# Kernel tuning notes

Hardware: AMD Instinct MI355X
Metric: run time of the kernel (lower is better)

## Reference

```python
import jax, jax.numpy as jnp
import numpy as np

TEMP = 1.0


def _layernorm(x):
    # mean/std over last dim; torch.std is unbiased (ddof=1); no eps in original
    x = x - jnp.mean(x, axis=-1, keepdims=True)
    return x / jnp.std(x, axis=-1, keepdims=True, ddof=1)


def setup_inputs() -> dict:
    key = jax.random.key(0)
    ks = jax.random.split(key, 5)
    B, S, d_in, d = 8, 2048, 768, 1024
    return {
        "seq": jax.random.normal(ks[0], (B, S, d_in), dtype=jnp.float32),
        "embedding": jax.random.normal(ks[1], (d_in, d), dtype=jnp.float32),
        "W1": jax.random.normal(ks[2], (d, d), dtype=jnp.float32),
        "W2": jax.random.normal(ks[3], (d, d), dtype=jnp.float32),
        "readout": jax.random.normal(ks[4], (d,), dtype=jnp.float32),
    }


def reference(seq, embedding, W1, W2, readout):
    d_in = seq.shape[-1]
    d = embedding.shape[-1]
    x = jnp.matmul(seq, embedding) / jnp.sqrt(jnp.float32(d_in))  # [B,S,d]
    # depth == 1: single block
    gram = jnp.einsum("bsd,btd->bst", x, x) / x.shape[-1]  # [B,S,S]
    weights = jax.nn.softmax(gram / TEMP, axis=-1)
    post_attn = _layernorm(x + jnp.matmul(weights, x))  # [B,S,d]
    h = jnp.matmul(post_attn, W1) / jnp.sqrt(jnp.float32(d))
    h = jnp.matmul(jax.nn.relu(h), W2) / jnp.sqrt(jnp.float32(d))
    x = _layernorm(h + post_attn)
    pooled = jnp.mean(x, axis=1)  # [B,d]
    out = jnp.matmul(pooled, readout) / jnp.sqrt(jnp.float32(d))  # [B]
    return out
```

## Files before the change

kernel.cpp:

```cpp
#include <hip/hip_runtime.h>
#include <hip/hip_bf16.h>

typedef __bf16 bf16x8 __attribute__((ext_vector_type(8)));
typedef float f32x4 __attribute__((ext_vector_type(4)));

__device__ __forceinline__ unsigned short f2bf(float f) {
  union { float f; unsigned u; } x; x.f = f;
  unsigned r = x.u + 0x7fffu + ((x.u >> 16) & 1u);
  return (unsigned short)(r >> 16);
}
__device__ __forceinline__ float bf2f(unsigned short u) {
  union { unsigned u; float f; } x; x.u = (unsigned)u << 16;
  return x.f;
}
__device__ __forceinline__ unsigned short f2h(float f) {
  union { _Float16 h; unsigned short u; } x; x.h = (_Float16)f;
  return x.u;
}
__device__ __forceinline__ float h2f(unsigned short u) {
  union { _Float16 h; unsigned short u; } x; x.u = u;
  return (float)x.h;
}

__device__ __forceinline__ void async_ld16(const void* g, void* l) {
  __builtin_amdgcn_global_load_lds(
      (__attribute__((address_space(1))) void*)const_cast<void*>(g),
      (__attribute__((address_space(3))) void*)l, 16, 0, 0);
}


#define EPI_F32    0
#define EPI_BF     1
#define EPI_RELUBF 2
#define EPI_F16    3

__global__ __launch_bounds__(512, 2) void gemm_bt(
    const unsigned short* __restrict__ A,
    const unsigned short* __restrict__ Bt,
    int M, int N, int K, int nbatch,
    long sA, long sB, long sC,
    float scale, int mode, void* __restrict__ outp)
{
  __shared__ unsigned short lds[65536];
  const int t = threadIdx.x;
  const int w = t >> 6, l = t & 63;
  const int lr = l & 15, lg = l >> 4;
  const int wr = w >> 2, wc = w & 3;
  const int ntn = N >> 8;
  const int tiles = (M >> 8) * ntn;
  const int chunk = (tiles * nbatch) >> 3;
  const int bid = blockIdx.x;
  const int wg = (bid & 7) * chunk + (bid >> 3);
  const int batch = wg / tiles;
  const int rem = wg - batch * tiles;
  const int row0 = (rem / ntn) << 8;
  const int col0 = (rem % ntn) << 8;

  const unsigned short* Ab  = A  + (long)batch * sA;
  const unsigned short* Btb = Bt + (long)batch * sB;

  const int ks = ((lg ^ ((lr >> 1) & 3)) << 3);

  const int srow = w * 16 + (l >> 2);
  const int kgo  = (((l & 3) ^ ((l >> 3) & 3)) << 3);
  const long aoff0 = (long)(row0 + srow) * K + kgo;
  const long boff0 = (long)(col0 + srow) * K + kgo;
  const long off128 = (long)K << 7;

  const int NT = K >> 6;

#define STAGEP(partE, base, kcol)                                      \
  { async_ld16((base) + (kcol),          &lds[(partE) + t * 8]);       \
    async_ld16((base) + off128 + (kcol), &lds[(partE) + 4096 + t * 8]); }

  f32x4 acc[8][4];
#pragma unroll
  for (int m = 0; m < 8; ++m)
#pragma unroll
    for (int n = 0; n < 4; ++n) acc[m][n] = (f32x4){0.f, 0.f, 0.f, 0.f};

  STAGEP(0,     Btb + boff0, 0);
  STAGEP(8192,  Ab + aoff0,  0);
  STAGEP(16384, Btb + boff0, 32);
  STAGEP(24576, Ab + aoff0,  32);
  __builtin_amdgcn_sched_barrier(0);

  for (int tt = 0; tt < NT; ++tt) {
    const int bufe  = (tt & 1) << 15;
    const int nbufe = ((tt + 1) & 1) << 15;
    const bool st = (tt + 1) < NT;
    const int kn = (tt + 1) << 6;

#pragma unroll
    for (int kh = 0; kh < 2; ++kh) {
      if (kh == 0 || st) { asm volatile("s_waitcnt vmcnt(4)" ::: "memory"); }
      else               { asm volatile("s_waitcnt vmcnt(0)" ::: "memory"); }
      __builtin_amdgcn_sched_barrier(0);
      __builtin_amdgcn_s_barrier();
      __builtin_amdgcn_sched_barrier(0);

      const int pB = bufe + kh * 16384;
      const int pA = pB + 8192;

      bf16x8 bfr[4];
#pragma unroll
      for (int nf = 0; nf < 4; ++nf) {
        int rb = wc * 64 + nf * 16 + lr;
        bfr[nf] = *(const bf16x8*)&lds[pB + rb * 32 + ks];
      }
      {
        bf16x8 af[4];
#pragma unroll
        for (int i = 0; i < 4; ++i) {
          int ra = wr * 128 + i * 16 + lr;
          af[i] = *(const bf16x8*)&lds[pA + ra * 32 + ks];
        }
        if (st) STAGEP(nbufe + kh * 16384, Btb + boff0, kn + kh * 32);
        __builtin_amdgcn_s_setprio(1);
#pragma unroll
        for (int i = 0; i < 4; ++i)
#pragma unroll
          for (int nf = 0; nf < 4; ++nf)
            acc[i][nf] = __builtin_amdgcn_mfma_f32_16x16x32_bf16(af[i], bfr[nf], acc[i][nf], 0, 0, 0);
        __builtin_amdgcn_s_setprio(0);
      }
      {
        bf16x8 af[4];
#pragma unroll
        for (int i = 0; i < 4; ++i) {
          int ra = wr * 128 + 64 + i * 16 + lr;
          af[i] = *(const bf16x8*)&lds[pA + ra * 32 + ks];
        }
        if (st) STAGEP(nbufe + kh * 16384 + 8192, Ab + aoff0, kn + kh * 32);
        __builtin_amdgcn_s_setprio(1);
#pragma unroll
        for (int i = 0; i < 4; ++i)
#pragma unroll
          for (int nf = 0; nf < 4; ++nf)
            acc[4 + i][nf] = __builtin_amdgcn_mfma_f32_16x16x32_bf16(af[i], bfr[nf], acc[4 + i][nf], 0, 0, 0);
        __builtin_amdgcn_s_setprio(0);
      }
      __builtin_amdgcn_sched_barrier(0);
    }
  }

  float* outF = (float*)outp;
  unsigned short* outH = (unsigned short*)outp;
  const size_t cb = (size_t)batch * (size_t)sC;
#pragma unroll
  for (int mf = 0; mf < 8; ++mf) {
    int rbase = row0 + wr * 128 + mf * 16 + lg * 4;
#pragma unroll
    for (int nf = 0; nf < 4; ++nf) {
      int c = col0 + wc * 64 + nf * 16 + lr;
      f32x4 v = acc[mf][nf];
#pragma unroll
      for (int q = 0; q < 4; ++q) {
        size_t idx = cb + (size_t)(rbase + q) * N + c;
        float val = v[q] * scale;
        if (mode == EPI_F32)         outF[idx] = val;
        else if (mode == EPI_BF)     outH[idx] = f2bf(val);
        else if (mode == EPI_RELUBF) outH[idx] = f2bf(fmaxf(val, 0.f));
        else                         outH[idx] = f2h(val);
      }
    }
  }
#undef STAGEP
}

__global__ __launch_bounds__(512, 2) void gram_sym(
    const unsigned short* __restrict__ X,
    unsigned short* __restrict__ outH)
{
  __shared__ unsigned short lds[65536];
  const int t = threadIdx.x;
  const int w = t >> 6, l = t & 63;
  const int lr = l & 15, lg = l >> 4;
  const int wr = w >> 2, wc = w & 3;
  const int bid = blockIdx.x;
  const int wg = (bid & 7) * 36 + (bid >> 3);
  const int batch = wg / 36;
  int r8 = wg - batch * 36;
  int bi = 0;
  while (r8 >= 8 - bi) { r8 -= 8 - bi; ++bi; }
  const int bj = bi + r8;
  const int row0 = bi << 8;
  const int col0 = bj << 8;

  const unsigned short* Xb = X + (long)batch * 2048 * 1024;

  const int ks = ((lg ^ ((lr >> 1) & 3)) << 3);
  const int srow = w * 16 + (l >> 2);
  const int kgo  = (((l & 3) ^ ((l >> 3) & 3)) << 3);
  const long aoff0 = (long)(row0 + srow) * 1024 + kgo;
  const long boff0 = (long)(col0 + srow) * 1024 + kgo;
  const long off128 = 1024L << 7;

#define STAGEP(partE, base, kcol)                                      \
  { async_ld16((base) + (kcol),          &lds[(partE) + t * 8]);       \
    async_ld16((base) + off128 + (kcol), &lds[(partE) + 4096 + t * 8]); }

  f32x4 acc[8][4];
#pragma unroll
  for (int m = 0; m < 8; ++m)
#pragma unroll
    for (int n = 0; n < 4; ++n) acc[m][n] = (f32x4){0.f, 0.f, 0.f, 0.f};

  STAGEP(0,     Xb + boff0, 0);
  STAGEP(8192,  Xb + aoff0,  0);
  STAGEP(16384, Xb + boff0, 32);
  STAGEP(24576, Xb + aoff0,  32);
  __builtin_amdgcn_sched_barrier(0);

  for (int tt = 0; tt < 16; ++tt) {
    const int bufe  = (tt & 1) << 15;
    const int nbufe = ((tt + 1) & 1) << 15;
    const bool st = (tt + 1) < 16;
    const int kn = (tt + 1) << 6;

#pragma unroll
    for (int kh = 0; kh < 2; ++kh) {
      if (kh == 0 || st) { asm volatile("s_waitcnt vmcnt(4)" ::: "memory"); }
      else               { asm volatile("s_waitcnt vmcnt(0)" ::: "memory"); }
      __builtin_amdgcn_sched_barrier(0);
      __builtin_amdgcn_s_barrier();
      __builtin_amdgcn_sched_barrier(0);

      const int pB = bufe + kh * 16384;
      const int pA = pB + 8192;

      bf16x8 bfr[4];
#pragma unroll
      for (int nf = 0; nf < 4; ++nf) {
        int rb = wc * 64 + nf * 16 + lr;
        bfr[nf] = *(const bf16x8*)&lds[pB + rb * 32 + ks];
      }
      {
        bf16x8 af[4];
#pragma unroll
        for (int i = 0; i < 4; ++i) {
          int ra = wr * 128 + i * 16 + lr;
          af[i] = *(const bf16x8*)&lds[pA + ra * 32 + ks];
        }
        if (st) STAGEP(nbufe + kh * 16384, Xb + boff0, kn + kh * 32);
        __builtin_amdgcn_s_setprio(1);
#pragma unroll
        for (int i = 0; i < 4; ++i)
#pragma unroll
          for (int nf = 0; nf < 4; ++nf)
            acc[i][nf] = __builtin_amdgcn_mfma_f32_16x16x32_bf16(af[i], bfr[nf], acc[i][nf], 0, 0, 0);
        __builtin_amdgcn_s_setprio(0);
      }
      {
        bf16x8 af[4];
#pragma unroll
        for (int i = 0; i < 4; ++i) {
          int ra = wr * 128 + 64 + i * 16 + lr;
          af[i] = *(const bf16x8*)&lds[pA + ra * 32 + ks];
        }
        if (st) STAGEP(nbufe + kh * 16384 + 8192, Xb + aoff0, kn + kh * 32);
        __builtin_amdgcn_s_setprio(1);
#pragma unroll
        for (int i = 0; i < 4; ++i)
#pragma unroll
          for (int nf = 0; nf < 4; ++nf)
            acc[4 + i][nf] = __builtin_amdgcn_mfma_f32_16x16x32_bf16(af[i], bfr[nf], acc[4 + i][nf], 0, 0, 0);
        __builtin_amdgcn_s_setprio(0);
      }
      __builtin_amdgcn_sched_barrier(0);
    }
  }

  unsigned short* ob = outH + (size_t)batch * 2048 * 2048;
  const float scale = 1.0f / 1024.0f;
  const bool mirror = (bi != bj);
#pragma unroll
  for (int mf = 0; mf < 8; ++mf) {
    int rbase = row0 + wr * 128 + mf * 16 + lg * 4;
#pragma unroll
    for (int nf = 0; nf < 4; ++nf) {
      int c = col0 + wc * 64 + nf * 16 + lr;
      f32x4 v = acc[mf][nf];
      unsigned short h0 = f2h(v[0] * scale), h1 = f2h(v[1] * scale);
      unsigned short h2 = f2h(v[2] * scale), h3 = f2h(v[3] * scale);
      ob[(size_t)(rbase + 0) * 2048 + c] = h0;
      ob[(size_t)(rbase + 1) * 2048 + c] = h1;
      ob[(size_t)(rbase + 2) * 2048 + c] = h2;
      ob[(size_t)(rbase + 3) * 2048 + c] = h3;
      if (mirror) {
        ushort4 m4 = {h0, h1, h2, h3};
        *(ushort4*)&ob[(size_t)c * 2048 + rbase] = m4;
      }
    }
  }
#undef STAGEP
}


__device__ __forceinline__ float wave_sum(float v) {
#pragma unroll
  for (int o = 32; o; o >>= 1) v += __shfl_xor(v, o, 64);
  return v;
}
__device__ __forceinline__ float wave_max(float v) {
#pragma unroll
  for (int o = 32; o; o >>= 1) v = fmaxf(v, __shfl_xor(v, o, 64));
  return v;
}

__global__ __launch_bounds__(256) void cast_bf16(const float* __restrict__ in,
                                                 unsigned short* __restrict__ out, long n) {
  long i = ((long)blockIdx.x * 256 + threadIdx.x) * 4;
  if (i >= n) return;
  float4 v = *(const float4*)&in[i];
  ushort4 o;
  o.x = f2bf(v.x); o.y = f2bf(v.y); o.z = f2bf(v.z); o.w = f2bf(v.w);
  *(ushort4*)&out[i] = o;
}

__global__ __launch_bounds__(256) void transpose_cast(const float* __restrict__ in,
                                                      unsigned short* __restrict__ out,
                                                      int R, int C) {
  __shared__ float tile[32][33];
  int c0 = blockIdx.x * 32, r0 = blockIdx.y * 32;
  int tx = threadIdx.x, ty = threadIdx.y;
  for (int i = ty; i < 32; i += 8) tile[i][tx] = in[(size_t)(r0 + i) * C + c0 + tx];
  __syncthreads();
  for (int i = ty; i < 32; i += 8) out[(size_t)(c0 + i) * R + r0 + tx] = f2bf(tile[tx][i]);
}

__global__ __launch_bounds__(256) void transpose_b16(const unsigned short* __restrict__ in,
                                                     unsigned short* __restrict__ out,
                                                     int R, int C) {
  __shared__ unsigned short tile[32][33];
  int c0 = blockIdx.x * 32, r0 = blockIdx.y * 32;
  size_t zb = (size_t)blockIdx.z * R * C;
  int tx = threadIdx.x, ty = threadIdx.y;
  for (int i = ty; i < 32; i += 8) tile[i][tx] = in[zb + (size_t)(r0 + i) * C + c0 + tx];
  __syncthreads();
  for (int i = ty; i < 32; i += 8) out[zb + (size_t)(c0 + i) * R + r0 + tx] = tile[tx][i];
}

__global__ __launch_bounds__(256) void softmax_rows(const unsigned short* __restrict__ g,
                                                    unsigned short* __restrict__ wout) {
  __shared__ float red[4];
  int row = blockIdx.x, t = threadIdx.x;
  const unsigned short* gr = g + ((size_t)row << 11) + t * 8;
  ushort4 ua = *(const ushort4*)gr;
  ushort4 ub = *(const ushort4*)(gr + 4);
  float a0 = h2f(ua.x), a1 = h2f(ua.y), a2 = h2f(ua.z), a3 = h2f(ua.w);
  float b0 = h2f(ub.x), b1 = h2f(ub.y), b2 = h2f(ub.z), b3 = h2f(ub.w);
  float mx = fmaxf(fmaxf(fmaxf(a0, a1), fmaxf(a2, a3)),
                   fmaxf(fmaxf(b0, b1), fmaxf(b2, b3)));
  mx = wave_max(mx);
  if ((t & 63) == 0) red[t >> 6] = mx;
  __syncthreads();
  mx = fmaxf(fmaxf(red[0], red[1]), fmaxf(red[2], red[3]));
  float e0 = __expf(a0 - mx), e1 = __expf(a1 - mx), e2 = __expf(a2 - mx), e3 = __expf(a3 - mx);
  float e4 = __expf(b0 - mx), e5 = __expf(b1 - mx), e6 = __expf(b2 - mx), e7 = __expf(b3 - mx);
  float s = ((e0 + e1) + (e2 + e3)) + ((e4 + e5) + (e6 + e7));
  s = wave_sum(s);
  __syncthreads();
  if ((t & 63) == 0) red[t >> 6] = s;
  __syncthreads();
  s = (red[0] + red[1]) + (red[2] + red[3]);
  float inv = 1.0f / s;
  ushort4 o0, o1;
  o0.x = f2bf(e0 * inv); o0.y = f2bf(e1 * inv); o0.z = f2bf(e2 * inv); o0.w = f2bf(e3 * inv);
  o1.x = f2bf(e4 * inv); o1.y = f2bf(e5 * inv); o1.z = f2bf(e6 * inv); o1.w = f2bf(e7 * inv);
  size_t base = ((size_t)row << 11) + t * 8;
  *(ushort4*)&wout[base] = o0;
  *(ushort4*)&wout[base + 4] = o1;
}

__global__ __launch_bounds__(256) void ln_residual_bb(const unsigned short* __restrict__ xb,
                                                      const unsigned short* __restrict__ ab,
                                                      unsigned short* __restrict__ outB) {
  __shared__ float red[4];
  int row = blockIdx.x, t = threadIdx.x;
  size_t base = ((size_t)row << 10) + t * 4;
  ushort4 ua = *(const ushort4*)&xb[base];
  ushort4 ub = *(const ushort4*)&ab[base];
  float4 v = {bf2f(ua.x) + bf2f(ub.x), bf2f(ua.y) + bf2f(ub.y),
              bf2f(ua.z) + bf2f(ub.z), bf2f(ua.w) + bf2f(ub.w)};
  float s = (v.x + v.y) + (v.z + v.w);
  float ss = (v.x * v.x + v.y * v.y) + (v.z * v.z + v.w * v.w);
  s = wave_sum(s);
  if ((t & 63) == 0) red[t >> 6] = s;
  __syncthreads();
  s = (red[0] + red[1]) + (red[2] + red[3]);
  ss = wave_sum(ss);
  __syncthreads();
  if ((t & 63) == 0) red[t >> 6] = ss;
  __syncthreads();
  ss = (red[0] + red[1]) + (red[2] + red[3]);
  float mean = s * (1.0f / 1024.0f);
  float var = (ss - s * mean) * (1.0f / 1023.0f);
  float rstd = rsqrtf(var);
  ushort4 ob;
  ob.x = f2bf((v.x - mean) * rstd); ob.y = f2bf((v.y - mean) * rstd);
  ob.z = f2bf((v.z - mean) * rstd); ob.w = f2bf((v.w - mean) * rstd);
  *(ushort4*)&outB[base] = ob;
}

__global__ __launch_bounds__(256) void ln_residual_dot(const unsigned short* __restrict__ h2,
                                                       const unsigned short* __restrict__ post,
                                                       const float* __restrict__ readout,
                                                       float* __restrict__ rowdot) {
  __shared__ float red[4];
  int row = blockIdx.x, t = threadIdx.x;
  size_t base = ((size_t)row << 10) + t * 4;
  ushort4 ua = *(const ushort4*)&h2[base];
  ushort4 ub = *(const ushort4*)&post[base];
  float4 v = {bf2f(ua.x) + bf2f(ub.x), bf2f(ua.y) + bf2f(ub.y),
              bf2f(ua.z) + bf2f(ub.z), bf2f(ua.w) + bf2f(ub.w)};
  float s = (v.x + v.y) + (v.z + v.w);
  float ss = (v.x * v.x + v.y * v.y) + (v.z * v.z + v.w * v.w);
  s = wave_sum(s);
  if ((t & 63) == 0) red[t >> 6] = s;
  __syncthreads();
  s = (red[0] + red[1]) + (red[2] + red[3]);
  ss = wave_sum(ss);
  __syncthreads();
  if ((t & 63) == 0) red[t >> 6] = ss;
  __syncthreads();
  ss = (red[0] + red[1]) + (red[2] + red[3]);
  float mean = s * (1.0f / 1024.0f);
  float var = (ss - s * mean) * (1.0f / 1023.0f);
  float rstd = rsqrtf(var);
  float4 r = *(const float4*)&readout[t * 4];
  float dot = (v.x - mean) * rstd * r.x + (v.y - mean) * rstd * r.y +
              (v.z - mean) * rstd * r.z + (v.w - mean) * rstd * r.w;
  dot = wave_sum(dot);
  __syncthreads();
  if ((t & 63) == 0) red[t >> 6] = dot;
  __syncthreads();
  if (t == 0) rowdot[row] = (red[0] + red[1]) + (red[2] + red[3]);
}

__global__ __launch_bounds__(256) void reduce_out(const float* __restrict__ rowdot,
                                                  float* __restrict__ out) {
  __shared__ float red[4];
  int b = blockIdx.x, t = threadIdx.x;
  float s = 0.f;
  for (int i = t; i < 2048; i += 256) s += rowdot[(size_t)b * 2048 + i];
  s = wave_sum(s);
  if ((t & 63) == 0) red[t >> 6] = s;
  __syncthreads();
  if (t == 0) out[b] = ((red[0] + red[1]) + (red[2] + red[3])) * (1.0f / 65536.0f);
}

extern "C" void kernel_launch(void* const* d_in, const int* in_sizes, int n_in,
                              void* d_out, int out_size, void* d_ws, size_t ws_size,
                              hipStream_t stream) {
  const float* seq     = (const float*)d_in[0];
  const float* emb     = (const float*)d_in[1];
  const float* W1      = (const float*)d_in[2];
  const float* W2      = (const float*)d_in[3];
  const float* readout = (const float*)d_in[4];
  float* out = (float*)d_out;

  char* ws = (char*)d_ws;
  const size_t MB = 1024u * 1024u;
  unsigned short* x_b    = (unsigned short*)(ws + 0);
  unsigned short* h2b    = (unsigned short*)(ws + 0);
  unsigned short* xT     = (unsigned short*)(ws + 32 * MB);
  unsigned short* hrelu  = (unsigned short*)(ws + 32 * MB);
  unsigned short* gram   = (unsigned short*)(ws + 64 * MB);
  unsigned short* attn_b = (unsigned short*)(ws + 64 * MB);
  unsigned short* wts    = (unsigned short*)(ws + 128 * MB);
  unsigned short* post_b = (unsigned short*)(ws + 128 * MB);
  unsigned short* seq_b  = (unsigned short*)(ws + 192 * MB);
  unsigned short* embT   = (unsigned short*)(ws + 216 * MB);
  unsigned short* W1T    = (unsigned short*)(ws + 218 * MB);
  unsigned short* W2T    = (unsigned short*)(ws + 220 * MB);
  float*          rowdot = (float*)(ws + 222 * MB);

  cast_bf16<<<12288, 256, 0, stream>>>(seq, seq_b, 12582912L);
  transpose_cast<<<dim3(32, 24), dim3(32, 8), 0, stream>>>(emb, embT, 768, 1024);
  transpose_cast<<<dim3(32, 32), dim3(32, 8), 0, stream>>>(W1, W1T, 1024, 1024);
  transpose_cast<<<dim3(32, 32), dim3(32, 8), 0, stream>>>(W2, W2T, 1024, 1024);

  gemm_bt<<<256, 512, 0, stream>>>(seq_b, embT, 16384, 1024, 768, 1, 0, 0, 0,
                                   0.03608439182435161f, EPI_BF, x_b);

  transpose_b16<<<dim3(32, 64, 8), dim3(32, 8), 0, stream>>>(x_b, xT, 2048, 1024);

  gram_sym<<<288, 512, 0, stream>>>(x_b, gram);

  softmax_rows<<<16384, 256, 0, stream>>>(gram, wts);

  gemm_bt<<<256, 512, 0, stream>>>(wts, xT, 2048, 1024, 2048, 8,
                                   2048L * 2048, 1024L * 2048, 2048L * 1024,
                                   1.0f, EPI_BF, attn_b);

  ln_residual_bb<<<16384, 256, 0, stream>>>(x_b, attn_b, post_b);

  gemm_bt<<<256, 512, 0, stream>>>(post_b, W1T, 16384, 1024, 1024, 1, 0, 0, 0,
                                   0.03125f, EPI_RELUBF, hrelu);
  gemm_bt<<<256, 512, 0, stream>>>(hrelu, W2T, 16384, 1024, 1024, 1, 0, 0, 0,
                                   0.03125f, EPI_BF, h2b);

  ln_residual_dot<<<16384, 256, 0, stream>>>(h2b, post_b, readout, rowdot);
  reduce_out<<<8, 256, 0, stream>>>(rowdot, out);
}
```

Measured before the change: 368.5 us.

## Fuse fp32-to-bf16 cast into embedding GEMM and retile symmetric gram kernel

```diff
diff --git a/kernel.cpp b/kernel.cpp
--- a/kernel.cpp
+++ b/kernel.cpp
@@ -28,6 +28,7 @@
       (__attribute__((address_space(3))) void*)l, 16, 0, 0);
 }
 
+#define SB __builtin_amdgcn_sched_barrier(0)
 
 #define EPI_F32    0
 #define EPI_BF     1
@@ -60,7 +61,6 @@
   const unsigned short* Btb = Bt + (long)batch * sB;
 
   const int ks = ((lg ^ ((lr >> 1) & 3)) << 3);
-
   const int srow = w * 16 + (l >> 2);
   const int kgo  = (((l & 3) ^ ((l >> 3) & 3)) << 3);
   const long aoff0 = (long)(row0 + srow) * K + kgo;
@@ -83,7 +83,7 @@
   STAGEP(8192,  Ab + aoff0,  0);
   STAGEP(16384, Btb + boff0, 32);
   STAGEP(24576, Ab + aoff0,  32);
-  __builtin_amdgcn_sched_barrier(0);
+  SB;
 
   for (int tt = 0; tt < NT; ++tt) {
     const int bufe  = (tt & 1) << 15;
@@ -95,9 +95,9 @@
     for (int kh = 0; kh < 2; ++kh) {
       if (kh == 0 || st) { asm volatile("s_waitcnt vmcnt(4)" ::: "memory"); }
       else               { asm volatile("s_waitcnt vmcnt(0)" ::: "memory"); }
-      __builtin_amdgcn_sched_barrier(0);
+      SB;
       __builtin_amdgcn_s_barrier();
-      __builtin_amdgcn_sched_barrier(0);
+      SB;
 
       const int pB = bufe + kh * 16384;
       const int pA = pB + 8192;
@@ -140,7 +140,7 @@
             acc[4 + i][nf] = __builtin_amdgcn_mfma_f32_16x16x32_bf16(af[i], bfr[nf], acc[4 + i][nf], 0, 0, 0);
         __builtin_amdgcn_s_setprio(0);
       }
-      __builtin_amdgcn_sched_barrier(0);
+      SB;
     }
   }
 
@@ -168,37 +168,46 @@
 #undef STAGEP
 }
 
-__global__ __launch_bounds__(512, 2) void gram_sym(
-    const unsigned short* __restrict__ X,
-    unsigned short* __restrict__ outH)
+__global__ __launch_bounds__(512, 2) void g1_fused(
+    const float* __restrict__ A,
+    const unsigned short* __restrict__ Bt,
+    float scale, unsigned short* __restrict__ outB)
 {
   __shared__ unsigned short lds[65536];
   const int t = threadIdx.x;
   const int w = t >> 6, l = t & 63;
   const int lr = l & 15, lg = l >> 4;
   const int wr = w >> 2, wc = w & 3;
+  const int K = 768;
   const int bid = blockIdx.x;
-  const int wg = (bid & 7) * 36 + (bid >> 3);
-  const int batch = wg / 36;
-  int r8 = wg - batch * 36;
-  int bi = 0;
-  while (r8 >= 8 - bi) { r8 -= 8 - bi; ++bi; }
-  const int bj = bi + r8;
-  const int row0 = bi << 8;
-  const int col0 = bj << 8;
-
-  const unsigned short* Xb = X + (long)batch * 2048 * 1024;
+  const int wg = (bid & 7) * 32 + (bid >> 3);
+  const int row0 = (wg >> 2) << 8;
+  const int col0 = (wg & 3) << 8;
 
   const int ks = ((lg ^ ((lr >> 1) & 3)) << 3);
   const int srow = w * 16 + (l >> 2);
   const int kgo  = (((l & 3) ^ ((l >> 3) & 3)) << 3);
-  const long aoff0 = (long)(row0 + srow) * 1024 + kgo;
-  const long boff0 = (long)(col0 + srow) * 1024 + kgo;
-  const long off128 = 1024L << 7;
-
-#define STAGEP(partE, base, kcol)                                      \
-  { async_ld16((base) + (kcol),          &lds[(partE) + t * 8]);       \
-    async_ld16((base) + off128 + (kcol), &lds[(partE) + 4096 + t * 8]); }
+  const long ar0 = (long)(row0 + srow) * K + kgo;
+  const long ar1 = ar0 + (long)128 * K;
+  const long boff0 = (long)(col0 + srow) * K + kgo;
+  const long off128 = (long)K << 7;
+  const int NT = 12;
+
+#define STAGEB(partE, kcol)                                              \
+  { async_ld16(Bt + boff0 + (kcol),          &lds[(partE) + t * 8]);     \
+    async_ld16(Bt + boff0 + off128 + (kcol), &lds[(partE) + 4096 + t * 8]); }
+#define WRA(partE, q0, q1, q2, q3)                                       \
+  { uint4 pk;                                                            \
+    pk.x = (unsigned)f2bf(q0.x) | ((unsigned)f2bf(q0.y) << 16);          \
+    pk.y = (unsigned)f2bf(q0.z) | ((unsigned)f2bf(q0.w) << 16);          \
+    pk.z = (unsigned)f2bf(q1.x) | ((unsigned)f2bf(q1.y) << 16);          \
+    pk.w = (unsigned)f2bf(q1.z) | ((unsigned)f2bf(q1.w) << 16);          \
+    *(uint4*)&lds[(partE) + t * 8] = pk;                                 \
+    pk.x = (unsigned)f2bf(q2.x) | ((unsigned)f2bf(q2.y) << 16);          \
+    pk.y = (unsigned)f2bf(q2.z) | ((unsigned)f2bf(q2.w) << 16);          \
+    pk.z = (unsigned)f2bf(q3.x) | ((unsigned)f2bf(q3.y) << 16);          \
+    pk.w = (unsigned)f2bf(q3.z) | ((unsigned)f2bf(q3.w) << 16);          \
+    *(uint4*)&lds[(partE) + 4096 + t * 8] = pk; }
 
   f32x4 acc[8][4];
 #pragma unroll
@@ -206,25 +215,31 @@
 #pragma unroll
     for (int n = 0; n < 4; ++n) acc[m][n] = (f32x4){0.f, 0.f, 0.f, 0.f};
 
-  STAGEP(0,     Xb + boff0, 0);
-  STAGEP(8192,  Xb + aoff0,  0);
-  STAGEP(16384, Xb + boff0, 32);
-  STAGEP(24576, Xb + aoff0,  32);
-  __builtin_amdgcn_sched_barrier(0);
-
-  for (int tt = 0; tt < 16; ++tt) {
+  float4 ap0, ap1, ap2, ap3, ap4, ap5, ap6, ap7;
+  ap0 = *(const float4*)&A[ar0];      ap1 = *(const float4*)&A[ar0 + 4];
+  ap2 = *(const float4*)&A[ar1];      ap3 = *(const float4*)&A[ar1 + 4];
+  ap4 = *(const float4*)&A[ar0 + 32]; ap5 = *(const float4*)&A[ar0 + 36];
+  ap6 = *(const float4*)&A[ar1 + 32]; ap7 = *(const float4*)&A[ar1 + 36];
+  STAGEB(0, 0);
+  STAGEB(16384, 32);
+  WRA(8192,  ap0, ap1, ap2, ap3);
+  WRA(24576, ap4, ap5, ap6, ap7);
+  SB;
+
+  for (int tt = 0; tt < NT; ++tt) {
     const int bufe  = (tt & 1) << 15;
     const int nbufe = ((tt + 1) & 1) << 15;
-    const bool st = (tt + 1) < 16;
+    const bool st = (tt + 1) < NT;
     const int kn = (tt + 1) << 6;
 
 #pragma unroll
     for (int kh = 0; kh < 2; ++kh) {
-      if (kh == 0 || st) { asm volatile("s_waitcnt vmcnt(4)" ::: "memory"); }
-      else               { asm volatile("s_waitcnt vmcnt(0)" ::: "memory"); }
-      __builtin_amdgcn_sched_barrier(0);
+      if (kh == 0)  { asm volatile("s_waitcnt vmcnt(2) lgkmcnt(0)" ::: "memory"); }
+      else if (st)  { asm volatile("s_waitcnt vmcnt(10) lgkmcnt(0)" ::: "memory"); }
+      else          { asm volatile("s_waitcnt vmcnt(0) lgkmcnt(0)" ::: "memory"); }
+      SB;
       __builtin_amdgcn_s_barrier();
-      __builtin_amdgcn_sched_barrier(0);
+      SB;
 
       const int pB = bufe + kh * 16384;
       const int pA = pB + 8192;
@@ -242,7 +257,13 @@
           int ra = wr * 128 + i * 16 + lr;
           af[i] = *(const bf16x8*)&lds[pA + ra * 32 + ks];
         }
-        if (st) STAGEP(nbufe + kh * 16384, Xb + boff0, kn + kh * 32);
+        if (kh == 0 && st) {
+          ap0 = *(const float4*)&A[ar0 + kn];      ap1 = *(const float4*)&A[ar0 + kn + 4];
+          ap2 = *(const float4*)&A[ar1 + kn];      ap3 = *(const float4*)&A[ar1 + kn + 4];
+          ap4 = *(const float4*)&A[ar0 + kn + 32]; ap5 = *(const float4*)&A[ar0 + kn + 36];
+          ap6 = *(const float4*)&A[ar1 + kn + 32]; ap7 = *(const float4*)&A[ar1 + kn + 36];
+          STAGEB(nbufe + 0, kn);
+        }
         __builtin_amdgcn_s_setprio(1);
 #pragma unroll
         for (int i = 0; i < 4; ++i)
@@ -258,7 +279,7 @@
           int ra = wr * 128 + 64 + i * 16 + lr;
           af[i] = *(const bf16x8*)&lds[pA + ra * 32 + ks];
         }
-        if (st) STAGEP(nbufe + kh * 16384 + 8192, Xb + aoff0, kn + kh * 32);
+        if (kh == 1 && st) STAGEB(nbufe + 16384, kn + 32);
         __builtin_amdgcn_s_setprio(1);
 #pragma unroll
         for (int i = 0; i < 4; ++i)
@@ -266,14 +287,15 @@
           for (int nf = 0; nf < 4; ++nf)
             acc[4 + i][nf] = __builtin_amdgcn_mfma_f32_16x16x32_bf16(af[i], bfr[nf], acc[4 + i][nf], 0, 0, 0);
         __builtin_amdgcn_s_setprio(0);
-      }
-      __builtin_amdgcn_sched_barrier(0);
+        if (kh == 1 && st) {
+          WRA(nbufe + 8192,  ap0, ap1, ap2, ap3);
+          WRA(nbufe + 24576, ap4, ap5, ap6, ap7);
+        }
+      }
+      SB;
     }
   }
 
-  unsigned short* ob = outH + (size_t)batch * 2048 * 2048;
-  const float scale = 1.0f / 1024.0f;
-  const bool mirror = (bi != bj);
 #pragma unroll
   for (int mf = 0; mf < 8; ++mf) {
     int rbase = row0 + wr * 128 + mf * 16 + lg * 4;
@@ -281,19 +303,129 @@
     for (int nf = 0; nf < 4; ++nf) {
       int c = col0 + wc * 64 + nf * 16 + lr;
       f32x4 v = acc[mf][nf];
+#pragma unroll
+      for (int q = 0; q < 4; ++q)
+        outB[(size_t)(rbase + q) * 1024 + c] = f2bf(v[q] * scale);
+    }
+  }
+#undef STAGEB
+#undef WRA
+}
+
+__global__ __launch_bounds__(512, 2) void gram_sym2(
+    const unsigned short* __restrict__ X,
+    unsigned short* __restrict__ outH)
+{
+  __shared__ unsigned short lds[49152];
+  const int t = threadIdx.x;
+  const int w = t >> 6, l = t & 63;
+  const int lr = l & 15, lg = l >> 4;
+  const int wr = w >> 2, wc = w & 3;
+  const int bid = blockIdx.x;
+  const int wg = (bid & 7) * 72 + (bid >> 3);
+  const int batch = wg / 72;
+  int f = wg - batch * 72;
+  int bi = 0;
+  while (f >= 8 - (bi >> 1)) { f -= 8 - (bi >> 1); ++bi; }
+  const int bj = (bi >> 1) + f;
+  const int row0 = bi << 7;
+  const int col0 = bj << 8;
+
+  const unsigned short* Xb = X + (long)batch * 2048 * 1024;
+
+  const int ks = ((lg ^ ((lr >> 1) & 3)) << 3);
+  const int srow = w * 16 + (l >> 2);
+  const int kgoB = (((l & 3) ^ ((l >> 3) & 3)) << 3);
+  const long boff0 = (long)(col0 + srow) * 1024 + kgoB;
+  const long off128 = 1024L << 7;
+  const long arow = (long)(row0 + (t >> 2)) * 1024 + (((t & 3) ^ ((t >> 3) & 3)) << 3);
+
+#define STAGEB2(partE, kcol)                                              \
+  { async_ld16(Xb + boff0 + (kcol),          &lds[(partE) + t * 8]);      \
+    async_ld16(Xb + boff0 + off128 + (kcol), &lds[(partE) + 4096 + t * 8]); }
+#define STAGEA2(partE, kcol)                                              \
+  { async_ld16(Xb + arow + (kcol), &lds[(partE) + t * 8]); }
+
+  f32x4 acc[4][4];
+#pragma unroll
+  for (int m = 0; m < 4; ++m)
+#pragma unroll
+    for (int n = 0; n < 4; ++n) acc[m][n] = (f32x4){0.f, 0.f, 0.f, 0.f};
+
+  STAGEB2(0, 0);
+  STAGEA2(8192, 0);
+  STAGEB2(12288, 32);
+  STAGEA2(20480, 32);
+  SB;
+
+  for (int tt = 0; tt < 16; ++tt) {
+    const int bufe  = (tt & 1) * 24576;
+    const int nbufe = ((tt + 1) & 1) * 24576;
+    const bool st = (tt + 1) < 16;
+    const int kn = (tt + 1) << 6;
+
+#pragma unroll
+    for (int kh = 0; kh < 2; ++kh) {
+      if (kh == 0 || st) { asm volatile("s_waitcnt vmcnt(3)" ::: "memory"); }
+      else               { asm volatile("s_waitcnt vmcnt(0)" ::: "memory"); }
+      SB;
+      __builtin_amdgcn_s_barrier();
+      SB;
+
+      const int pB = bufe + kh * 12288;
+      const int pA = pB + 8192;
+
+      bf16x8 bfr[4];
+#pragma unroll
+      for (int nf = 0; nf < 4; ++nf) {
+        int rb = wc * 64 + nf * 16 + lr;
+        bfr[nf] = *(const bf16x8*)&lds[pB + rb * 32 + ks];
+      }
+#pragma unroll
+      for (int mh = 0; mh < 2; ++mh) {
+        bf16x8 af[2];
+#pragma unroll
+        for (int i = 0; i < 2; ++i) {
+          int ra = wr * 64 + mh * 32 + i * 16 + lr;
+          af[i] = *(const bf16x8*)&lds[pA + ra * 32 + ks];
+        }
+        if (st) {
+          if (mh == 0) { if (kh == 0) STAGEB2(nbufe + 0, kn) else STAGEB2(nbufe + 12288, kn + 32) }
+          else         { if (kh == 0) STAGEA2(nbufe + 8192, kn) else STAGEA2(nbufe + 20480, kn + 32) }
+        }
+        __builtin_amdgcn_s_setprio(1);
+#pragma unroll
+        for (int i = 0; i < 2; ++i)
+#pragma unroll
+          for (int nf = 0; nf < 4; ++nf)
+            acc[mh * 2 + i][nf] = __builtin_amdgcn_mfma_f32_16x16x32_bf16(af[i], bfr[nf], acc[mh * 2 + i][nf], 0, 0, 0);
+        __builtin_amdgcn_s_setprio(0);
+      }
+      SB;
+    }
+  }
+
+  unsigned short* ob = outH + (size_t)batch * 2048 * 2048;
+  const float scale = 1.0f / 1024.0f;
+#pragma unroll
+  for (int am = 0; am < 4; ++am) {
+    int rbase = row0 + wr * 64 + (am >> 1) * 32 + (am & 1) * 16 + lg * 4;
+#pragma unroll
+    for (int nf = 0; nf < 4; ++nf) {
+      int c = col0 + wc * 64 + nf * 16 + lr;
+      f32x4 v = acc[am][nf];
       unsigned short h0 = f2h(v[0] * scale), h1 = f2h(v[1] * scale);
       unsigned short h2 = f2h(v[2] * scale), h3 = f2h(v[3] * scale);
       ob[(size_t)(rbase + 0) * 2048 + c] = h0;
       ob[(size_t)(rbase + 1) * 2048 + c] = h1;
       ob[(size_t)(rbase + 2) * 2048 + c] = h2;
       ob[(size_t)(rbase + 3) * 2048 + c] = h3;
-      if (mirror) {
-        ushort4 m4 = {h0, h1, h2, h3};
-        *(ushort4*)&ob[(size_t)c * 2048 + rbase] = m4;
-      }
+      ushort4 m4 = {h0, h1, h2, h3};
+      *(ushort4*)&ob[(size_t)c * 2048 + rbase] = m4;
     }
   }
-#undef STAGEP
+#undef STAGEB2
+#undef STAGEA2
 }
 
 
@@ -306,16 +438,6 @@
 #pragma unroll
   for (int o = 32; o; o >>= 1) v = fmaxf(v, __shfl_xor(v, o, 64));
   return v;
-}
-
-__global__ __launch_bounds__(256) void cast_bf16(const float* __restrict__ in,
-                                                 unsigned short* __restrict__ out, long n) {
-  long i = ((long)blockIdx.x * 256 + threadIdx.x) * 4;
-  if (i >= n) return;
-  float4 v = *(const float4*)&in[i];
-  ushort4 o;
-  o.x = f2bf(v.x); o.y = f2bf(v.y); o.z = f2bf(v.z); o.w = f2bf(v.w);
-  *(ushort4*)&out[i] = o;
 }
 
 __global__ __launch_bounds__(256) void transpose_cast(const float* __restrict__ in,
@@ -470,23 +592,20 @@
   unsigned short* attn_b = (unsigned short*)(ws + 64 * MB);
   unsigned short* wts    = (unsigned short*)(ws + 128 * MB);
   unsigned short* post_b = (unsigned short*)(ws + 128 * MB);
-  unsigned short* seq_b  = (unsigned short*)(ws + 192 * MB);
   unsigned short* embT   = (unsigned short*)(ws + 216 * MB);
   unsigned short* W1T    = (unsigned short*)(ws + 218 * MB);
   unsigned short* W2T    = (unsigned short*)(ws + 220 * MB);
   float*          rowdot = (float*)(ws + 222 * MB);
 
-  cast_bf16<<<12288, 256, 0, stream>>>(seq, seq_b, 12582912L);
   transpose_cast<<<dim3(32, 24), dim3(32, 8), 0, stream>>>(emb, embT, 768, 1024);
   transpose_cast<<<dim3(32, 32), dim3(32, 8), 0, stream>>>(W1, W1T, 1024, 1024);
   transpose_cast<<<dim3(32, 32), dim3(32, 8), 0, stream>>>(W2, W2T, 1024, 1024);
 
-  gemm_bt<<<256, 512, 0, stream>>>(seq_b, embT, 16384, 1024, 768, 1, 0, 0, 0,
-                                   0.03608439182435161f, EPI_BF, x_b);
+  g1_fused<<<256, 512, 0, stream>>>(seq, embT, 0.03608439182435161f, x_b);
 
   transpose_b16<<<dim3(32, 64, 8), dim3(32, 8), 0, stream>>>(x_b, xT, 2048, 1024);
 
-  gram_sym<<<288, 512, 0, stream>>>(x_b, gram);
+  gram_sym2<<<576, 512, 0, stream>>>(x_b, gram);
 
   softmax_rows<<<16384, 256, 0, stream>>>(gram, wts);
 
```

Measured after the change: 359.8 us. 2.4% less time.
